# Optimization experiments

Hardware: AMD Instinct MI355X
Metric: run time of the kernel (lower is better)

Reference implementation:

```python
import jax, jax.numpy as jnp
import numpy as np

N_NODES = 100000


def setup_inputs() -> dict:
    key = jax.random.key(0)
    k1, k2, k3, k4, k5 = jax.random.split(key, 5)
    d_in, d_out, n_edges = 128, 128, 640000
    x = jax.random.normal(k1, (N_NODES, d_in), dtype=jnp.float32)
    edge_index = jax.random.randint(k2, (2, n_edges), 0, N_NODES, dtype=jnp.int64)
    # uniform(size, W) in the source is U(-1/sqrt(in), 1/sqrt(in)); scaled normal is fine as data
    s = 1.0 / np.sqrt(d_in)
    Wc = jax.random.normal(k3, (d_in, d_out), dtype=jnp.float32) * s
    Wn = jax.random.normal(k4, (d_in, d_out), dtype=jnp.float32) * s
    b = jax.random.normal(k5, (d_out,), dtype=jnp.float32) * s
    return {"x": x, "edge_index": edge_index, "Wc": Wc, "Wn": Wn, "b": b}


def reference(x, edge_index, Wc, Wn, b):
    row, col = edge_index[0], edge_index[1]
    alpha = x @ Wc                      # [N, out]
    beta = x @ Wn                       # [N, out]
    # Vectorized scatter-mean replacing the original per-node Python loop:
    # gamma[n] = mean(beta[col[row == n]])
    num = jax.ops.segment_sum(beta[col], row, num_segments=N_NODES)   # [N, out]
    cnt = jax.ops.segment_sum(jnp.ones_like(row, dtype=beta.dtype), row, num_segments=N_NODES)
    gamma = num / jnp.maximum(cnt, 1.0)[:, None]  # NOTE: unused below, exactly as in the original forward
    del gamma
    # The original returns alpha + beta + bias (gamma is dead code in the source).
    return alpha + beta + b
```

## Files before the change

### kernel.cpp

```cpp
#include <hip/hip_runtime.h>
#include <hip/hip_bf16.h>


#define NROWS 100000

typedef __attribute__((ext_vector_type(8))) __bf16 bf16x8;
typedef __attribute__((ext_vector_type(8))) unsigned short u16x8;
typedef __attribute__((ext_vector_type(4))) float f32x4;

__device__ __forceinline__ bf16x8 pack8(const float4 lo, const float4 hi) {
    bf16x8 r;
    r[0] = (__bf16)lo.x; r[1] = (__bf16)lo.y; r[2] = (__bf16)lo.z; r[3] = (__bf16)lo.w;
    r[4] = (__bf16)hi.x; r[5] = (__bf16)hi.y; r[6] = (__bf16)hi.z; r[7] = (__bf16)hi.w;
    return r;
}

__global__ void prep_wt(const float* __restrict__ Wc, const float* __restrict__ Wn,
                        __bf16* __restrict__ wt) {
    int i = blockIdx.x * 256 + threadIdx.x;
    int n = i >> 7, k = i & 127;
    wt[i] = (__bf16)(Wc[k * 128 + n] + Wn[k * 128 + n]);
}

__global__ __launch_bounds__(256) void gemm_bias(
    const float* __restrict__ x, const __bf16* __restrict__ wt,
    const float* __restrict__ bias_g, float* __restrict__ out) {

    __shared__ __align__(16) __bf16 sWt[128 * 136];

    const int tid = threadIdx.x;
    #pragma unroll
    for (int it = 0; it < 8; ++it) {
        int idx8 = it * 256 + tid;
        int n = idx8 >> 4;
        int k = (idx8 & 15) << 3;
        *(bf16x8*)&sWt[n * 136 + k] = *(const bf16x8*)(wt + (idx8 << 3));
    }
    __syncthreads();

    const int wave = tid >> 6;
    const int lane = tid & 63;
    const int quad = lane >> 4;
    const int l16  = lane & 15;

    const long rowbase = (long)blockIdx.x * 128 + wave * 32;
    if (rowbase >= NROWS) return;

    f32x4 bv[8];
    #pragma unroll
    for (int ct = 0; ct < 8; ++ct)
        bv[ct] = *(const f32x4*)(bias_g + ct * 16 + quad * 4);

    f32x4 acc[2][8] = {};

    const float* xr0 = x + (rowbase + l16) * 128;
    const float* xr1 = xr0 + 16 * 128;

    #pragma unroll
    for (int kc = 0; kc < 4; ++kc) {
        const int ko = kc * 32 + quad * 8;
        float4 b0lo = *(const float4*)(xr0 + ko);
        float4 b0hi = *(const float4*)(xr0 + ko + 4);
        float4 b1lo = *(const float4*)(xr1 + ko);
        float4 b1hi = *(const float4*)(xr1 + ko + 4);
        bf16x8 xb0 = pack8(b0lo, b0hi);
        bf16x8 xb1 = pack8(b1lo, b1hi);
        #pragma unroll
        for (int ct = 0; ct < 8; ++ct) {
            bf16x8 wa = *(const bf16x8*)&sWt[(ct * 16 + l16) * 136 + ko];
            acc[0][ct] = __builtin_amdgcn_mfma_f32_16x16x32_bf16(wa, xb0, acc[0][ct], 0, 0, 0);
            acc[1][ct] = __builtin_amdgcn_mfma_f32_16x16x32_bf16(wa, xb1, acc[1][ct], 0, 0, 0);
        }
    }

    #pragma unroll
    for (int g = 0; g < 2; ++g) {
        float* orow = out + (rowbase + g * 16 + l16) * 128 + quad * 4;
        #pragma unroll
        for (int ct = 0; ct < 8; ++ct) {
            f32x4 v = acc[g][ct] + bv[ct];
            __builtin_nontemporal_store(v, (f32x4*)(orow + ct * 16));
        }
    }
}

extern "C" void kernel_launch(void* const* d_in, const int* in_sizes, int n_in,
                              void* d_out, int out_size, void* d_ws, size_t ws_size,
                              hipStream_t stream) {
    const float* x  = (const float*)d_in[0];
    const float* Wc = (const float*)d_in[2];
    const float* Wn = (const float*)d_in[3];
    const float* b  = (const float*)d_in[4];
    __bf16* wt = (__bf16*)d_ws;
    float* out = (float*)d_out;

    prep_wt<<<64, 256, 0, stream>>>(Wc, Wn, wt);
    const int nblocks = (NROWS + 127) / 128;
    gemm_bias<<<nblocks, 256, 0, stream>>>(x, wt, b, out);
}
```

Measured before the change: 116.7 us.

## Fuse weight prep into GEMM kernel and prefetch x before weight staging

Removes the separate prep_wt launch. Each block now reads Wc and Wn directly, sums them, converts to bf16 and transposes into shared memory. The x row loads are issued before the weight staging, so their global latency overlaps the shared-memory fill, and bias loads move into the epilogue. The cost is that every one of the ~782 blocks reads 128 KB of fp32 weights instead of 32 KB of bf16, and the transposed scalar bf16 stores to shared memory may cause bank conflicts.

```diff
diff --git a/kernel.cpp b/kernel.cpp
--- a/kernel.cpp
+++ b/kernel.cpp
@@ -5,7 +5,6 @@
 #define NROWS 100000
 
 typedef __attribute__((ext_vector_type(8))) __bf16 bf16x8;
-typedef __attribute__((ext_vector_type(8))) unsigned short u16x8;
 typedef __attribute__((ext_vector_type(4))) float f32x4;
 
 __device__ __forceinline__ bf16x8 pack8(const float4 lo, const float4 hi) {
@@ -15,61 +14,58 @@
     return r;
 }
 
-__global__ void prep_wt(const float* __restrict__ Wc, const float* __restrict__ Wn,
-                        __bf16* __restrict__ wt) {
-    int i = blockIdx.x * 256 + threadIdx.x;
-    int n = i >> 7, k = i & 127;
-    wt[i] = (__bf16)(Wc[k * 128 + n] + Wn[k * 128 + n]);
-}
-
-__global__ __launch_bounds__(256) void gemm_bias(
-    const float* __restrict__ x, const __bf16* __restrict__ wt,
-    const float* __restrict__ bias_g, float* __restrict__ out) {
+__global__ __launch_bounds__(256) void fout_fused(
+    const float* __restrict__ x, const float* __restrict__ Wc,
+    const float* __restrict__ Wn, const float* __restrict__ bias_g,
+    float* __restrict__ out) {
 
     __shared__ __align__(16) __bf16 sWt[128 * 136];
 
-    const int tid = threadIdx.x;
-    #pragma unroll
-    for (int it = 0; it < 8; ++it) {
-        int idx8 = it * 256 + tid;
-        int n = idx8 >> 4;
-        int k = (idx8 & 15) << 3;
-        *(bf16x8*)&sWt[n * 136 + k] = *(const bf16x8*)(wt + (idx8 << 3));
-    }
-    __syncthreads();
-
+    const int tid  = threadIdx.x;
     const int wave = tid >> 6;
     const int lane = tid & 63;
     const int quad = lane >> 4;
     const int l16  = lane & 15;
 
     const long rowbase = (long)blockIdx.x * 128 + wave * 32;
-    if (rowbase >= NROWS) return;
+    const bool valid = rowbase < NROWS;
 
-    f32x4 bv[8];
-    #pragma unroll
-    for (int ct = 0; ct < 8; ++ct)
-        bv[ct] = *(const f32x4*)(bias_g + ct * 16 + quad * 4);
+    bf16x8 xb[2][4];
+    if (valid) {
+        const float* xr0 = x + (rowbase + l16) * 128;
+        const float* xr1 = xr0 + 16 * 128;
+        #pragma unroll
+        for (int kc = 0; kc < 4; ++kc) {
+            const int ko = kc * 32 + quad * 8;
+            xb[0][kc] = pack8(*(const float4*)(xr0 + ko), *(const float4*)(xr0 + ko + 4));
+            xb[1][kc] = pack8(*(const float4*)(xr1 + ko), *(const float4*)(xr1 + ko + 4));
+        }
+    }
+
+    const float4* Wc4 = (const float4*)Wc;
+    const float4* Wn4 = (const float4*)Wn;
+    #pragma unroll 4
+    for (int it = 0; it < 16; ++it) {
+        const int f = it * 256 + tid;
+        const int k = f >> 5, n4 = f & 31;
+        float4 a = Wc4[f], b = Wn4[f];
+        sWt[(n4 * 4 + 0) * 136 + k] = (__bf16)(a.x + b.x);
+        sWt[(n4 * 4 + 1) * 136 + k] = (__bf16)(a.y + b.y);
+        sWt[(n4 * 4 + 2) * 136 + k] = (__bf16)(a.z + b.z);
+        sWt[(n4 * 4 + 3) * 136 + k] = (__bf16)(a.w + b.w);
+    }
+    __syncthreads();
+    if (!valid) return;
 
     f32x4 acc[2][8] = {};
-
-    const float* xr0 = x + (rowbase + l16) * 128;
-    const float* xr1 = xr0 + 16 * 128;
-
     #pragma unroll
     for (int kc = 0; kc < 4; ++kc) {
         const int ko = kc * 32 + quad * 8;
-        float4 b0lo = *(const float4*)(xr0 + ko);
-        float4 b0hi = *(const float4*)(xr0 + ko + 4);
-        float4 b1lo = *(const float4*)(xr1 + ko);
-        float4 b1hi = *(const float4*)(xr1 + ko + 4);
-        bf16x8 xb0 = pack8(b0lo, b0hi);
-        bf16x8 xb1 = pack8(b1lo, b1hi);
         #pragma unroll
         for (int ct = 0; ct < 8; ++ct) {
             bf16x8 wa = *(const bf16x8*)&sWt[(ct * 16 + l16) * 136 + ko];
-            acc[0][ct] = __builtin_amdgcn_mfma_f32_16x16x32_bf16(wa, xb0, acc[0][ct], 0, 0, 0);
-            acc[1][ct] = __builtin_amdgcn_mfma_f32_16x16x32_bf16(wa, xb1, acc[1][ct], 0, 0, 0);
+            acc[0][ct] = __builtin_amdgcn_mfma_f32_16x16x32_bf16(wa, xb[0][kc], acc[0][ct], 0, 0, 0);
+            acc[1][ct] = __builtin_amdgcn_mfma_f32_16x16x32_bf16(wa, xb[1][kc], acc[1][ct], 0, 0, 0);
         }
     }
 
@@ -78,7 +74,8 @@
         float* orow = out + (rowbase + g * 16 + l16) * 128 + quad * 4;
         #pragma unroll
         for (int ct = 0; ct < 8; ++ct) {
-            f32x4 v = acc[g][ct] + bv[ct];
+            f32x4 bv = *(const f32x4*)(bias_g + ct * 16 + quad * 4);
+            f32x4 v = acc[g][ct] + bv;
             __builtin_nontemporal_store(v, (f32x4*)(orow + ct * 16));
         }
     }
@@ -91,10 +88,8 @@
     const float* Wc = (const float*)d_in[2];
     const float* Wn = (const float*)d_in[3];
     const float* b  = (const float*)d_in[4];
-    __bf16* wt = (__bf16*)d_ws;
     float* out = (float*)d_out;
 
-    prep_wt<<<64, 256, 0, stream>>>(Wc, Wn, wt);
     const int nblocks = (NROWS + 127) / 128;
-    gemm_bias<<<nblocks, 256, 0, stream>>>(x, wt, b, out);
+    fout_fused<<<nblocks, 256, 0, stream>>>(x, Wc, Wn, b, out);
 }
```

Result: slower. 126.9 us (+8.7%).
